# Kernel tuning notes

Hardware: AMD Instinct MI355X
Metric: run time of the kernel (lower is better)

Reference implementation:

```python
import jax, jax.numpy as jnp
import numpy as np


def _conv(x, w, b, pad):
    # x: [N,C,H,W], w: [O,C,kh,kw]
    out = jax.lax.conv_general_dilated(
        x, w, window_strides=(1, 1), padding=[(pad, pad), (pad, pad)],
        dimension_numbers=("NCHW", "OIHW", "NCHW"))
    return out + b[None, :, None, None]


def _deform_conv(x, offset, mask, w, b):
    # Modulated deformable conv (DCNv2), 3x3 kernel, stride 1, pad 1, dilation 1.
    # x: [N,C,H,W], offset: [N,18,H,W] (per-point (dy,dx) pairs), mask: [N,9,H,W]
    N, C, H, W = x.shape
    KK = 9
    off = offset.reshape(N, KK, 2, H, W)
    dy, dx = off[:, :, 0], off[:, :, 1]            # [N,9,H,W]
    k = jnp.arange(3, dtype=x.dtype) - 1.0         # kernel taps -1,0,1
    ky = jnp.repeat(k, 3)                          # row-major 3x3 order
    kx = jnp.tile(k, 3)
    py = dy + ky[None, :, None, None] + jnp.arange(H, dtype=x.dtype)[None, None, :, None]
    px = dx + kx[None, :, None, None] + jnp.arange(W, dtype=x.dtype)[None, None, None, :]
    y0 = jnp.floor(py)
    x0 = jnp.floor(px)
    wy = (py - y0)[..., None]                      # [N,9,H,W,1]
    wx = (px - x0)[..., None]
    x_t = x.transpose(0, 2, 3, 1).reshape(N, H * W, C)  # [N,HW,C]

    def gather(iy, ix):
        valid = ((iy >= 0) & (iy < H) & (ix >= 0) & (ix < W)).astype(x.dtype)
        idx = (jnp.clip(iy, 0, H - 1).astype(jnp.int32) * W
               + jnp.clip(ix, 0, W - 1).astype(jnp.int32)).reshape(N, -1)
        v = jax.vmap(lambda a, i: a[i])(x_t, idx).reshape(N, KK, H, W, C)
        return v * valid[..., None]

    v00 = gather(y0, x0)
    v01 = gather(y0, x0 + 1)
    v10 = gather(y0 + 1, x0)
    v11 = gather(y0 + 1, x0 + 1)
    samp = (v00 * (1 - wy) * (1 - wx) + v01 * (1 - wy) * wx
            + v10 * wy * (1 - wx) + v11 * wy * wx)
    samp = samp * mask[..., None]                  # modulation
    O = w.shape[0]
    out = jnp.einsum("nkhwc,ock->nohw", samp, w.reshape(O, C, KK))
    return out + b[None, :, None, None]


def _res_block(x, w1, b1, w2, b2):
    # ResidualBlock_noBN: x + conv2(relu(conv1(x)))
    return x + _conv(jax.nn.relu(_conv(x, w1, b1, 1)), w2, b2, 1)


def setup_inputs() -> dict:
    key = jax.random.key(0)
    ks = jax.random.split(key, 16)
    f = jnp.float32

    def rn(k, shape, scale):
        return jax.random.normal(k, shape, dtype=f) * scale

    N, C, H, W = 2, 64, 128, 128
    inp = {}
    inp["xd"] = rn(ks[0], (N, 2 * C, H // 2, W // 2), 1.0)
    inp["xl"] = rn(ks[1], (N, C, H, W), 1.0)
    inp["xr"] = rn(ks[2], (N, C, H, W), 1.0)
    inp["up_w"] = rn(ks[3], (C, 2 * C, 2, 2), (2 * C * 4) ** -0.5)
    inp["up_b"] = jnp.zeros((C,), f)
    inp["offl_w"] = rn(ks[4], (27, 3 * C, 3, 3), 0.01 * (3 * C * 9) ** -0.5)
    inp["offl_b"] = jnp.zeros((27,), f)
    inp["dl_w"] = rn(ks[5], (C, C, 3, 3), (C * 9) ** -0.5)
    inp["dl_b"] = jnp.zeros((C,), f)
    inp["offr_w"] = rn(ks[6], (27, 3 * C, 3, 3), 0.01 * (3 * C * 9) ** -0.5)
    inp["offr_b"] = jnp.zeros((27,), f)
    inp["dr_w"] = rn(ks[7], (C, C, 3, 3), (C * 9) ** -0.5)
    inp["dr_b"] = jnp.zeros((C,), f)
    inp["cv_w"] = rn(ks[8], (C, 3 * C, 3, 3), (3 * C * 9) ** -0.5)
    inp["cv_b"] = jnp.zeros((C,), f)
    for i, nm in enumerate(["rb1_w1", "rb1_w2", "rb2_w1", "rb2_w2"]):
        inp[nm] = rn(ks[9 + i], (C, C, 3, 3), (C * 9) ** -0.5)
    for nm in ["rb1_b1", "rb1_b2", "rb2_b1", "rb2_b2"]:
        inp[nm] = jnp.zeros((C,), f)
    return inp


def reference(xd, xl, xr, up_w, up_b, offl_w, offl_b, dl_w, dl_b,
              offr_w, offr_b, dr_w, dr_b, cv_w, cv_b,
              rb1_w1, rb1_b1, rb1_w2, rb1_b2,
              rb2_w1, rb2_b1, rb2_w2, rb2_b2):
    # UP_SAMPLE: nearest x2 upsample, then k=2 conv (pad 0 -> size 2H-1)
    xd = jnp.repeat(jnp.repeat(xd, 2, axis=2), 2, axis=3)
    xd = _conv(xd, up_w, up_b, 0)
    dY = xl.shape[2] - xd.shape[2]
    dX = xl.shape[3] - xd.shape[3]
    xd = jnp.pad(xd, ((0, 0), (0, 0), (dY // 2, dY - dY // 2), (dX // 2, dX - dX // 2)))
    # left deform branch
    ol = _conv(jnp.concatenate([xl, xr, xd], axis=1), offl_w, offl_b, 1)
    off_l = ol[:, :18]                    # cat(o1, o2)
    mask_l = jax.nn.sigmoid(ol[:, 18:])
    xl = _deform_conv(xl, off_l, mask_l, dl_w, dl_b)
    # right deform branch (uses updated xl)
    orr = _conv(jnp.concatenate([xl, xr, xd], axis=1), offr_w, offr_b, 1)
    off_r = orr[:, :18]
    mask_r = jax.nn.sigmoid(orr[:, 18:])
    xr = _deform_conv(xr, off_r, mask_r, dr_w, dr_b)
    # CONV_BLOCK: conv+relu then two residual blocks
    x = jnp.concatenate([xl, xr, xd], axis=1)
    x = jax.nn.relu(_conv(x, cv_w, cv_b, 1))
    x = _res_block(x, rb1_w1, rb1_b1, rb1_w2, rb1_b2)
    x = _res_block(x, rb2_w1, rb2_b1, rb2_w2, rb2_b2)
    return x
```

## Files before the change

### kernel.cpp

```cpp
#include <hip/hip_runtime.h>
#include <math.h>

#define HW 16384

typedef unsigned short u16;
typedef __attribute__((ext_vector_type(8))) short short8;
typedef __attribute__((ext_vector_type(16))) float f32x16;

union U16B {
  uint4 u;
  short8 v;
  u16 s[8];
};

__device__ inline u16 f2b(float f) {
  unsigned u = __float_as_uint(f);
  u += 0x7FFF + ((u >> 16) & 1);
  return (u16)(u >> 16);
}
__device__ inline float b2f(u16 h) {
  return __uint_as_float(((unsigned)h) << 16);
}

__device__ inline u16 pack_frag(const float* __restrict__ w, int Cin, int O,
                                int OT, int d) {
  int j = d & 7;
  int lane = (d >> 3) & 63;
  int rest = d >> 9;
  int ot = rest % OT; rest /= OT;
  int ks = rest & 3; rest >>= 2;
  int kx = rest % 3; rest /= 3;
  int ky = rest % 3; int s = rest / 3;
  int och = ot * 32 + (lane & 31);
  int ch = s * 64 + ks * 16 + ((lane >> 5) << 3) + j;
  if (och >= O) return 0;
  return f2b(w[((size_t)och * Cin + ch) * 9 + ky * 3 + kx]);
}

__device__ inline u16 pack_def(const float* __restrict__ w, int d) {
  int j = d & 7;
  int lane = (d >> 3) & 63;
  int g = d >> 9;
  int ot = g & 1;
  int t = g >> 1;
  int ks = t & 3;
  int k = t >> 2;
  int och = ot * 32 + (lane & 31);
  int c = ks * 16 + ((lane >> 5) << 3) + j;
  return f2b(w[((size_t)och * 64 + c) * 9 + k]);
}

__device__ inline u16 pack_up(const float* __restrict__ w, int d) {
  int j = d & 7;
  int lane = (d >> 3) & 63;
  int g = d >> 9;
  int ot = g & 1;
  int rest = g >> 1;
  int ks = rest & 7;
  int t = rest >> 3;
  int och = ot * 32 + (lane & 31);
  int ci = ks * 16 + ((lane >> 5) << 3) + j;
  return f2b(w[((size_t)och * 128 + ci) * 4 + t]);
}

__global__ __launch_bounds__(256) void setup_kernel(
    const float* __restrict__ dl_w, const float* __restrict__ dr_w,
    const float* __restrict__ up_w, const float* __restrict__ cv_w,
    const float* __restrict__ offl_w, const float* __restrict__ offr_w,
    const float* __restrict__ r1a, const float* __restrict__ r1b,
    const float* __restrict__ r2a, const float* __restrict__ r2b,
    u16* __restrict__ wup, u16* __restrict__ wdl, u16* __restrict__ wdr,
    u16* __restrict__ wcv, u16* __restrict__ wofl, u16* __restrict__ wofr,
    u16* __restrict__ wr1a, u16* __restrict__ wr1b,
    u16* __restrict__ wr2a, u16* __restrict__ wr2b,
    const float* __restrict__ xl, const float* __restrict__ xr,
    u16* __restrict__ xlh, u16* __restrict__ xrh,
    const float* __restrict__ xd, u16* __restrict__ xdh) {
  __shared__ float sT[8448];
  int tid = threadIdx.x;
  int b = blockIdx.x;
  if (b < 1856) {
    int d = b * 256 + tid;
    if (d < 32768) { wup[d] = pack_up(up_w, d); return; }
    d -= 32768;
    if (d < 36864) { wdl[d] = pack_def(dl_w, d); return; }
    d -= 36864;
    if (d < 36864) { wdr[d] = pack_def(dr_w, d); return; }
    d -= 36864;
    if (d < 110592) { wcv[d] = pack_frag(cv_w, 192, 64, 2, d); return; }
    d -= 110592;
    if (d < 55296) { wofl[d] = pack_frag(offl_w, 192, 27, 1, d); return; }
    d -= 55296;
    if (d < 55296) { wofr[d] = pack_frag(offr_w, 192, 27, 1, d); return; }
    d -= 55296;
    if (d < 36864) { wr1a[d] = pack_frag(r1a, 64, 64, 2, d); return; }
    d -= 36864;
    if (d < 36864) { wr1b[d] = pack_frag(r1b, 64, 64, 2, d); return; }
    d -= 36864;
    if (d < 36864) { wr2a[d] = pack_frag(r2a, 64, 64, 2, d); return; }
    d -= 36864;
    if (d < 36864) { wr2b[d] = pack_frag(r2b, 64, 64, 2, d); return; }
    return;
  }
  b -= 1856;
  if (b < 512) {
    int y = b & 127;
    int pid = b >> 7;
    const float* src = (pid >> 1) ? xr : xl;
    u16* dst = (pid >> 1) ? xrh : xlh;
    int n = pid & 1;
#pragma unroll
    for (int i = 0; i < 8; ++i) {
      int q = tid + i * 256;
      int ch = q >> 5, pxq = q & 31;
      float4 v = *(const float4*)(src + ((size_t)(n * 64 + ch)) * HW + y * 128 + pxq * 4);
      *(float4*)&sT[ch * 132 + pxq * 4] = v;
    }
    __syncthreads();
    int px = tid >> 1, half = tid & 1;
    u16* op = dst + (((size_t)(n * 128 + y)) * 128 + px) * 64 + half * 32;
#pragma unroll
    for (int c = 0; c < 4; ++c) {
      uint4 v;
      int ob = (half * 32 + c * 8);
      v.x = (unsigned)f2b(sT[(ob + 0) * 132 + px]) | ((unsigned)f2b(sT[(ob + 1) * 132 + px]) << 16);
      v.y = (unsigned)f2b(sT[(ob + 2) * 132 + px]) | ((unsigned)f2b(sT[(ob + 3) * 132 + px]) << 16);
      v.z = (unsigned)f2b(sT[(ob + 4) * 132 + px]) | ((unsigned)f2b(sT[(ob + 5) * 132 + px]) << 16);
      v.w = (unsigned)f2b(sT[(ob + 6) * 132 + px]) | ((unsigned)f2b(sT[(ob + 7) * 132 + px]) << 16);
      *(uint4*)(op + c * 8) = v;
    }
    return;
  }
  b -= 512;
  {
    int r = b & 63;
    int n = b >> 6;
#pragma unroll
    for (int i = 0; i < 8; ++i) {
      int q = tid + i * 256;
      int ch = q >> 4, col4 = q & 15;
      float4 v = *(const float4*)(xd + ((size_t)(n * 128 + ch) * 64 + r) * 64 + col4 * 4);
      *(float4*)&sT[ch * 66 + col4 * 4] = v;
    }
    __syncthreads();
#pragma unroll
    for (int i = 0; i < 4; ++i) {
      int q = tid + i * 256;
      int col = q >> 4, cho = q & 15;
      uint4 v;
      int cb = cho * 8;
      v.x = (unsigned)f2b(sT[(cb + 0) * 66 + col]) | ((unsigned)f2b(sT[(cb + 1) * 66 + col]) << 16);
      v.y = (unsigned)f2b(sT[(cb + 2) * 66 + col]) | ((unsigned)f2b(sT[(cb + 3) * 66 + col]) << 16);
      v.z = (unsigned)f2b(sT[(cb + 4) * 66 + col]) | ((unsigned)f2b(sT[(cb + 5) * 66 + col]) << 16);
      v.w = (unsigned)f2b(sT[(cb + 6) * 66 + col]) | ((unsigned)f2b(sT[(cb + 7) * 66 + col]) << 16);
      *(uint4*)(xdh + (((size_t)(n * 64 + r)) * 64 + col) * 128 + cb) = v;
    }
  }
}

__global__ __launch_bounds__(1024) void upconv_mf(
    const u16* __restrict__ xdh, const u16* __restrict__ wup,
    const float* __restrict__ bias, u16* __restrict__ outH) {
  __shared__ float s_red[4][3][16][64];
  const int tid = threadIdx.x;
  const int lane = tid & 63;
  const int w = tid >> 6;
  const int p2 = w >> 2;
  const int t = w & 3;
  const int y = blockIdx.x;
  const int n = blockIdx.y;
  const int px = (p2 << 5) + (lane & 31);
  const int h = lane >> 5;

  f32x16 acc0, acc1;
#pragma unroll
  for (int i = 0; i < 16; ++i) { acc0[i] = 0.f; acc1[i] = 0.f; }

  const u16* xb = xdh + ((size_t)n * 64 * 64) * 128;
  const int ty = t >> 1, tx = t & 1;
  const int row = min((y + ty) >> 1, 63);
  const int col = min((px + tx) >> 1, 63);
  const u16* src = xb + ((size_t)(row * 64 + col)) * 128;
#pragma unroll
  for (int ks = 0; ks < 8; ++ks) {
    U16B bf;
    bf.u = *(const uint4*)(src + ks * 16 + h * 8);
    const u16* wp = wup + ((size_t)((t * 8 + ks) * 2)) * 512 + lane * 8;
    U16B a0, a1;
    a0.u = *(const uint4*)wp;
    a1.u = *(const uint4*)(wp + 512);
    acc0 = __builtin_amdgcn_mfma_f32_32x32x16_bf16(a0.v, bf.v, acc0, 0, 0, 0);
    acc1 = __builtin_amdgcn_mfma_f32_32x32x16_bf16(a1.v, bf.v, acc1, 0, 0, 0);
  }

  const bool zero = (y == 127) || (px == 127);
  const size_t pixb = (((size_t)(n * 128 + y)) * 128 + px) * 64;

  if (t != 0) {
#pragma unroll
    for (int i = 0; i < 16; ++i) s_red[p2][t - 1][i][lane] = acc0[i];
  }
  __syncthreads();
  if (t == 0) {
#pragma unroll
    for (int q = 0; q < 4; ++q) {
      int oo = 8 * q + 4 * h;
      float v[4];
#pragma unroll
      for (int r = 0; r < 4; ++r) {
        int i = q * 4 + r;
        float s = acc0[i] + s_red[p2][0][i][lane] + s_red[p2][1][i][lane] +
                  s_red[p2][2][i][lane];
        v[r] = zero ? 0.f : (s + bias[oo + r]);
      }
      ushort4 hh;
      hh.x = f2b(v[0]); hh.y = f2b(v[1]); hh.z = f2b(v[2]); hh.w = f2b(v[3]);
      *(ushort4*)(outH + pixb + oo) = hh;
    }
  }
  __syncthreads();
  if (t != 0) {
#pragma unroll
    for (int i = 0; i < 16; ++i) s_red[p2][t - 1][i][lane] = acc1[i];
  }
  __syncthreads();
  if (t == 0) {
#pragma unroll
    for (int q = 0; q < 4; ++q) {
      int oo = 32 + 8 * q + 4 * h;
      float v[4];
#pragma unroll
      for (int r = 0; r < 4; ++r) {
        int i = q * 4 + r;
        float s = acc1[i] + s_red[p2][0][i][lane] + s_red[p2][1][i][lane] +
                  s_red[p2][2][i][lane];
        v[r] = zero ? 0.f : (s + bias[oo + r]);
      }
      ushort4 hh;
      hh.x = f2b(v[0]); hh.y = f2b(v[1]); hh.z = f2b(v[2]); hh.w = f2b(v[3]);
      *(ushort4*)(outH + pixb + oo) = hh;
    }
  }
}

template <int NSEG>
__global__ __launch_bounds__(1024) void mfconv_s(
    const u16* __restrict__ in0, const u16* __restrict__ in1,
    const u16* __restrict__ in2, const u16* __restrict__ wpk,
    const float* __restrict__ bias, const u16* __restrict__ resh,
    float* __restrict__ outF, u16* __restrict__ outH, int mode) {
  __shared__ __align__(16) unsigned char s_un[49920];
  u16* stg = (u16*)s_un;
  float* s_redf = (float*)s_un;

  const int tid = threadIdx.x;
  const int lane = tid & 63;
  const int w = tid >> 6;
  const int p2 = w >> 2;
  const int kq = w & 3;
  const int y = blockIdx.x;
  const int n = blockIdx.y;
  const int px = (p2 << 5) + (lane & 31);
  const int h = lane >> 5;
  const int gpx = lane >> 3;
  const int gcs = lane & 7;

  auto stg_at = [&](int e, int cg, int p) -> u16* {
    return stg + (((e * 8 + cg) * 130 + p) << 3);
  };

  f32x16 acc0, acc1;
#pragma unroll
  for (int i = 0; i < 16; ++i) { acc0[i] = 0.f; acc1[i] = 0.f; }

  for (int s = 0; s < NSEG; ++s) {
    const u16* sp = (s == 0) ? in0 : ((s == 1) ? in1 : in2);
    const u16* bn = sp + ((size_t)n * 128) * 128 * 64;
    for (int i = w; i < 48; i += 16) {
      int ky = i >> 4, g = i & 15;
      int row = y + ky - 1;
      int ppx = g * 8 + gpx;
      uint4 v = make_uint4(0, 0, 0, 0);
      if ((unsigned)row < 128u)
        v = *(const uint4*)(bn + (size_t)row * (128 * 64) + (size_t)ppx * 64 + gcs * 8);
      *(uint4*)stg_at(ky, gcs, ppx) = v;
    }
    __syncthreads();
#pragma unroll
    for (int ky = 0; ky < 3; ++ky) {
#pragma unroll
      for (int kx = 0; kx < 3; ++kx) {
        int pxc = px + kx - 1;
        bool valid = (unsigned)pxc < 128u;
        int pxcc = min(max(pxc, 0), 127);
        U16B bf;
        bf.u = *(const uint4*)stg_at(ky, kq * 2 + h, pxcc);
        if (!valid) bf.u = make_uint4(0, 0, 0, 0);
        const u16* wp = wpk +
            ((size_t)((((s * 3 + ky) * 3 + kx) * 4 + kq) * 2)) * 512 + lane * 8;
        U16B a0, a1;
        a0.u = *(const uint4*)wp;
        a1.u = *(const uint4*)(wp + 512);
        acc0 = __builtin_amdgcn_mfma_f32_32x32x16_bf16(a0.v, bf.v, acc0, 0, 0, 0);
        acc1 = __builtin_amdgcn_mfma_f32_32x32x16_bf16(a1.v, bf.v, acc1, 0, 0, 0);
      }
    }
    __syncthreads();
  }

  const size_t pixb = ((size_t)(n * 128 + y)) * 128 + px;

  if (kq != 0) {
#pragma unroll
    for (int i = 0; i < 16; ++i)
      s_redf[((p2 * 3 + (kq - 1)) * 16 + i) * 64 + lane] = acc0[i];
  }
  __syncthreads();
  if (kq == 0) {
#pragma unroll
    for (int q = 0; q < 4; ++q) {
      int oo = 8 * q + 4 * h;
      float v[4];
#pragma unroll
      for (int r = 0; r < 4; ++r) {
        int i = q * 4 + r;
        v[r] = acc0[i] + s_redf[((p2 * 3 + 0) * 16 + i) * 64 + lane] +
               s_redf[((p2 * 3 + 1) * 16 + i) * 64 + lane] +
               s_redf[((p2 * 3 + 2) * 16 + i) * 64 + lane] + bias[oo + r];
      }
      if (mode == 1) {
#pragma unroll
        for (int r = 0; r < 4; ++r) v[r] = fmaxf(v[r], 0.f);
      } else if (mode == 3) {
        ushort4 rv = *(const ushort4*)(resh + pixb * 64 + oo);
        v[0] += b2f(rv.x); v[1] += b2f(rv.y); v[2] += b2f(rv.z); v[3] += b2f(rv.w);
      }
      if (outH) {
        ushort4 hh;
        hh.x = f2b(v[0]); hh.y = f2b(v[1]); hh.z = f2b(v[2]); hh.w = f2b(v[3]);
        *(ushort4*)(outH + pixb * 64 + oo) = hh;
      } else {
#pragma unroll
        for (int r = 0; r < 4; ++r)
          outF[((size_t)(n * 64 + oo + r)) * HW + y * 128 + px] = v[r];
      }
    }
  }
  __syncthreads();
  if (kq != 0) {
#pragma unroll
    for (int i = 0; i < 16; ++i)
      s_redf[((p2 * 3 + (kq - 1)) * 16 + i) * 64 + lane] = acc1[i];
  }
  __syncthreads();
  if (kq == 0) {
#pragma unroll
    for (int q = 0; q < 4; ++q) {
      int oo = 32 + 8 * q + 4 * h;
      float v[4];
#pragma unroll
      for (int r = 0; r < 4; ++r) {
        int i = q * 4 + r;
        v[r] = acc1[i] + s_redf[((p2 * 3 + 0) * 16 + i) * 64 + lane] +
               s_redf[((p2 * 3 + 1) * 16 + i) * 64 + lane] +
               s_redf[((p2 * 3 + 2) * 16 + i) * 64 + lane] + bias[oo + r];
      }
      if (mode == 1) {
#pragma unroll
        for (int r = 0; r < 4; ++r) v[r] = fmaxf(v[r], 0.f);
      } else if (mode == 3) {
        ushort4 rv = *(const ushort4*)(resh + pixb * 64 + oo);
        v[0] += b2f(rv.x); v[1] += b2f(rv.y); v[2] += b2f(rv.z); v[3] += b2f(rv.w);
      }
      if (outH) {
        ushort4 hh;
        hh.x = f2b(v[0]); hh.y = f2b(v[1]); hh.z = f2b(v[2]); hh.w = f2b(v[3]);
        *(ushort4*)(outH + pixb * 64 + oo) = hh;
      } else {
#pragma unroll
        for (int r = 0; r < 4; ++r)
          outF[((size_t)(n * 64 + oo + r)) * HW + y * 128 + px] = v[r];
      }
    }
  }
}

__global__ __launch_bounds__(512) void rbfuse(
    const u16* __restrict__ in, const u16* __restrict__ w1,
    const float* __restrict__ b1, const u16* __restrict__ w2,
    const float* __restrict__ b2, float* __restrict__ outF,
    u16* __restrict__ outH) {
  __shared__ __align__(16) u16 ring[3][8][128][8];
  __shared__ __align__(16) u16 mid[3][8][128][8];
  const int tid = threadIdx.x;
  const int lane = tid & 63;
  const int w = tid >> 6;
  const int p2 = w >> 1;
  const int ot = w & 1;
  const int y = blockIdx.x;
  const int n = blockIdx.y;
  const int px = (p2 << 5) + (lane & 31);
  const int h = lane >> 5;
  const int gpx = lane >> 3;
  const int gcs = lane & 7;
  const u16* bn = in + ((size_t)n * 128) * 128 * 64;

  auto stage_row = [&](int r) {
    int sl = ((r % 3) + 3) % 3;
    for (int i = w; i < 16; i += 8) {
      int ppx = i * 8 + gpx;
      uint4 v = make_uint4(0, 0, 0, 0);
      if ((unsigned)r < 128u)
        v = *(const uint4*)(bn + (size_t)r * (128 * 64) + (size_t)ppx * 64 + gcs * 8);
      *(uint4*)&ring[sl][gcs][ppx][0] = v;
    }
  };

  auto conv1_row = [&](int rr, int r) {
    if ((unsigned)r >= 128u) {
      ushort4 z = make_ushort4(0, 0, 0, 0);
#pragma unroll
      for (int q = 0; q < 4; ++q)
        *(ushort4*)&mid[rr][ot * 4 + q][px][4 * h] = z;
      return;
    }
    f32x16 acc;
#pragma unroll
    for (int i = 0; i < 16; ++i) acc[i] = 0.f;
#pragma unroll
    for (int ky = 0; ky < 3; ++ky) {
      int sr = r - 1 + ky;
      int sl = ((sr % 3) + 3) % 3;
#pragma unroll
      for (int kx = 0; kx < 3; ++kx) {
        int pxc = px + kx - 1;
        bool valid = (unsigned)pxc < 128u;
        int pxcc = min(max(pxc, 0), 127);
#pragma unroll
        for (int kq = 0; kq < 4; ++kq) {
          U16B bf;
          bf.u = *(const uint4*)&ring[sl][kq * 2 + h][pxcc][0];
          if (!valid) bf.u = make_uint4(0, 0, 0, 0);
          U16B a;
          a.u = *(const uint4*)(w1 +
                ((size_t)(((ky * 3 + kx) * 4 + kq) * 2 + ot)) * 512 + lane * 8);
          acc = __builtin_amdgcn_mfma_f32_32x32x16_bf16(a.v, bf.v, acc, 0, 0, 0);
        }
      }
    }
#pragma unroll
    for (int q = 0; q < 4; ++q) {
      int oo = ot * 32 + 8 * q + 4 * h;
      ushort4 hh;
      hh.x = f2b(fmaxf(acc[q * 4 + 0] + b1[oo + 0], 0.f));
      hh.y = f2b(fmaxf(acc[q * 4 + 1] + b1[oo + 1], 0.f));
      hh.z = f2b(fmaxf(acc[q * 4 + 2] + b1[oo + 2], 0.f));
      hh.w = f2b(fmaxf(acc[q * 4 + 3] + b1[oo + 3], 0.f));
      *(ushort4*)&mid[rr][ot * 4 + q][px][4 * h] = hh;
    }
  };

  stage_row(y - 2);
  stage_row(y - 1);
  stage_row(y);
  __syncthreads();
  conv1_row(0, y - 1);
  __syncthreads();
  stage_row(y + 1);
  __syncthreads();
  conv1_row(1, y);
  __syncthreads();
  stage_row(y + 2);
  __syncthreads();
  conv1_row(2, y + 1);
  __syncthreads();

  f32x16 acc;
#pragma unroll
  for (int i = 0; i < 16; ++i) acc[i] = 0.f;
#pragma unroll
  for (int ky = 0; ky < 3; ++ky) {
#pragma unroll
    for (int kx = 0; kx < 3; ++kx) {
      int pxc = px + kx - 1;
      bool valid = (unsigned)pxc < 128u;
      int pxcc = min(max(pxc, 0), 127);
#pragma unroll
      for (int kq = 0; kq < 4; ++kq) {
        U16B bf;
        bf.u = *(const uint4*)&mid[ky][kq * 2 + h][pxcc][0];
        if (!valid) bf.u = make_uint4(0, 0, 0, 0);
        U16B a;
        a.u = *(const uint4*)(w2 +
              ((size_t)(((ky * 3 + kx) * 4 + kq) * 2 + ot)) * 512 + lane * 8);
        acc = __builtin_amdgcn_mfma_f32_32x32x16_bf16(a.v, bf.v, acc, 0, 0, 0);
      }
    }
  }

  const int ysl = y % 3;
  const size_t pixb = ((size_t)(n * 128 + y)) * 128 + px;
#pragma unroll
  for (int q = 0; q < 4; ++q) {
    int oo = ot * 32 + 8 * q + 4 * h;
    ushort4 rv = *(const ushort4*)&ring[ysl][ot * 4 + q][px][4 * h];
    float v[4];
    v[0] = acc[q * 4 + 0] + b2[oo + 0] + b2f(rv.x);
    v[1] = acc[q * 4 + 1] + b2[oo + 1] + b2f(rv.y);
    v[2] = acc[q * 4 + 2] + b2[oo + 2] + b2f(rv.z);
    v[3] = acc[q * 4 + 3] + b2[oo + 3] + b2f(rv.w);
    if (outH) {
      ushort4 hh;
      hh.x = f2b(v[0]); hh.y = f2b(v[1]); hh.z = f2b(v[2]); hh.w = f2b(v[3]);
      *(ushort4*)(outH + pixb * 64 + oo) = hh;
    } else {
#pragma unroll
      for (int r = 0; r < 4; ++r)
        outF[((size_t)(n * 64 + oo + r)) * HW + y * 128 + px] = v[r];
    }
  }
}

__global__ __launch_bounds__(512) void deform_fused(
    const u16* __restrict__ in0, const u16* __restrict__ in1,
    const u16* __restrict__ in2, const u16* __restrict__ woff,
    const float* __restrict__ boff, const u16* __restrict__ xh,
    const u16* __restrict__ wdef, const float* __restrict__ bdef,
    u16* __restrict__ outH) {
  __shared__ float s_off[27][64];
  __shared__ __align__(16) unsigned char s_un[30720];
  u16* stg = (u16*)s_un;
  float* s_redf = (float*)s_un;

  const int tid = threadIdx.x;
  const int lane = tid & 63;
  const int w = tid >> 6;
  const int p2 = w >> 2;
  const int kq = w & 3;
  const int y = blockIdx.x >> 1;
  const int hx0 = (blockIdx.x & 1) << 6;
  const int n = blockIdx.y;
  const int lp = (p2 << 5) + (lane & 31);
  const int h = lane >> 5;
  const int gpx = lane >> 3;
  const int gcs = lane & 7;

  auto stg_at = [&](int e, int cg, int p) -> u16* {
    return stg + (((e * 8 + cg) * 80 + p) << 3);
  };

  f32x16 acc;
#pragma unroll
  for (int i = 0; i < 16; ++i) acc[i] = 0.f;

  for (int s = 0; s < 3; ++s) {
    const u16* sp = (s == 0) ? in0 : ((s == 1) ? in1 : in2);
    const u16* bn = sp + ((size_t)n * 128) * 128 * 64;
    for (int i = w; i < 30; i += 8) {
      int ky = i / 10, g = i % 10;
      int row = y + ky - 1;
      int ppx = hx0 - 8 + g * 8 + gpx;
      uint4 v = make_uint4(0, 0, 0, 0);
      if ((unsigned)row < 128u && (unsigned)ppx < 128u)
        v = *(const uint4*)(bn + (size_t)row * (128 * 64) + (size_t)ppx * 64 + gcs * 8);
      *(uint4*)stg_at(ky, gcs, g * 8 + gpx) = v;
    }
    __syncthreads();
#pragma unroll
    for (int ky = 0; ky < 3; ++ky) {
#pragma unroll
      for (int kx = 0; kx < 3; ++kx) {
        U16B bf;
        bf.u = *(const uint4*)stg_at(ky, kq * 2 + h, lp + 7 + kx);
        U16B a;
        a.u = *(const uint4*)(woff +
              ((size_t)(((s * 3 + ky) * 3 + kx) * 4 + kq)) * 512 + lane * 8);
        acc = __builtin_amdgcn_mfma_f32_32x32x16_bf16(a.v, bf.v, acc, 0, 0, 0);
      }
    }
    __syncthreads();
  }

  if (kq != 0) {
#pragma unroll
    for (int i = 0; i < 16; ++i)
      s_redf[((p2 * 3 + (kq - 1)) * 16 + i) * 64 + lane] = acc[i];
  }
  __syncthreads();
  if (kq == 0) {
#pragma unroll
    for (int q = 0; q < 4; ++q) {
#pragma unroll
      for (int r = 0; r < 4; ++r) {
        int och = 8 * q + 4 * h + r;
        if (och < 27) {
          int i = q * 4 + r;
          float v = acc[i] + s_redf[((p2 * 3 + 0) * 16 + i) * 64 + lane] +
                    s_redf[((p2 * 3 + 1) * 16 + i) * 64 + lane] +
                    s_redf[((p2 * 3 + 2) * 16 + i) * 64 + lane] + boff[och];
          if (och >= 18) v = 1.f / (1.f + expf(-v));
          s_off[och][lp] = v;
        }
      }
    }
  }
  __syncthreads();

  f32x16 acc0, acc1;
#pragma unroll
  for (int i = 0; i < 16; ++i) { acc0[i] = 0.f; acc1[i] = 0.f; }

  const u16* xb = xh + ((size_t)n * HW) * 64;

  for (int tc = 0; tc < 3; ++tc) {
    for (int i = w; i < 24; i += 8) {
      int tt = i >> 3, g = i & 7;
      int t = tc * 3 + tt;
      int ppx = g * 8 + gpx;
      int gx = hx0 + ppx;
      int ky = t / 3 - 1, kx = t % 3 - 1;
      float dy = s_off[2 * t][ppx];
      float dx = s_off[2 * t + 1][ppx];
      float m = s_off[18 + t][ppx];
      float py = dy + (float)(y + ky);
      float pxf = dx + (float)(gx + kx);
      float fy = floorf(py), fxx = floorf(pxf);
      float wy = py - fy, wx = pxf - fxx;
      int iy0 = (int)fy, ix0 = (int)fxx;
      bool vy0 = (unsigned)iy0 < 128u, vy1 = (unsigned)(iy0 + 1) < 128u;
      bool vx0 = (unsigned)ix0 < 128u, vx1 = (unsigned)(ix0 + 1) < 128u;
      float omwy = 1.f - wy, omwx = 1.f - wx;
      float f00 = (vy0 && vx0) ? omwy * omwx * m : 0.f;
      float f01 = (vy0 && vx1) ? omwy * wx * m : 0.f;
      float f10 = (vy1 && vx0) ? wy * omwx * m : 0.f;
      float f11 = (vy1 && vx1) ? wy * wx * m : 0.f;
      int y0c = min(max(iy0, 0), 127), y1c = min(max(iy0 + 1, 0), 127);
      int x0c = min(max(ix0, 0), 127), x1c = min(max(ix0 + 1, 0), 127);
      U16B v00, v01, v10, v11;
      v00.u = *(const uint4*)(xb + ((size_t)(y0c * 128 + x0c)) * 64 + gcs * 8);
      v01.u = *(const uint4*)(xb + ((size_t)(y0c * 128 + x1c)) * 64 + gcs * 8);
      v10.u = *(const uint4*)(xb + ((size_t)(y1c * 128 + x0c)) * 64 + gcs * 8);
      v11.u = *(const uint4*)(xb + ((size_t)(y1c * 128 + x1c)) * 64 + gcs * 8);
      unsigned dw[4];
#pragma unroll
      for (int jj = 0; jj < 4; ++jj) {
        float s0 = f00 * b2f(v00.s[2 * jj]) + f01 * b2f(v01.s[2 * jj]) +
                   f10 * b2f(v10.s[2 * jj]) + f11 * b2f(v11.s[2 * jj]);
        float s1 = f00 * b2f(v00.s[2 * jj + 1]) + f01 * b2f(v01.s[2 * jj + 1]) +
                   f10 * b2f(v10.s[2 * jj + 1]) + f11 * b2f(v11.s[2 * jj + 1]);
        dw[jj] = (unsigned)f2b(s0) | ((unsigned)f2b(s1) << 16);
      }
      *(uint4*)stg_at(tt, gcs, ppx) = make_uint4(dw[0], dw[1], dw[2], dw[3]);
    }
    __syncthreads();
#pragma unroll
    for (int tt = 0; tt < 3; ++tt) {
      int t = tc * 3 + tt;
      U16B bf;
      bf.u = *(const uint4*)stg_at(tt, kq * 2 + h, lp);
      const u16* wp = wdef + ((size_t)((t * 4 + kq) * 2)) * 512 + lane * 8;
      U16B a0, a1;
      a0.u = *(const uint4*)wp;
      a1.u = *(const uint4*)(wp + 512);
      acc0 = __builtin_amdgcn_mfma_f32_32x32x16_bf16(a0.v, bf.v, acc0, 0, 0, 0);
      acc1 = __builtin_amdgcn_mfma_f32_32x32x16_bf16(a1.v, bf.v, acc1, 0, 0, 0);
    }
    __syncthreads();
  }

  const size_t pixb = (((size_t)(n * 128 + y)) * 128 + hx0 + lp) * 64;
  if (kq != 0) {
#pragma unroll
    for (int i = 0; i < 16; ++i)
      s_redf[((p2 * 3 + (kq - 1)) * 16 + i) * 64 + lane] = acc0[i];
  }
  __syncthreads();
  if (kq == 0) {
#pragma unroll
    for (int q = 0; q < 4; ++q) {
      int oo = 8 * q + 4 * h;
      float v[4];
#pragma unroll
      for (int r = 0; r < 4; ++r) {
        int i = q * 4 + r;
        v[r] = acc0[i] + s_redf[((p2 * 3 + 0) * 16 + i) * 64 + lane] +
               s_redf[((p2 * 3 + 1) * 16 + i) * 64 + lane] +
               s_redf[((p2 * 3 + 2) * 16 + i) * 64 + lane] + bdef[oo + r];
      }
      ushort4 hh;
      hh.x = f2b(v[0]); hh.y = f2b(v[1]); hh.z = f2b(v[2]); hh.w = f2b(v[3]);
      *(ushort4*)(outH + pixb + oo) = hh;
    }
  }
  __syncthreads();
  if (kq != 0) {
#pragma unroll
    for (int i = 0; i < 16; ++i)
      s_redf[((p2 * 3 + (kq - 1)) * 16 + i) * 64 + lane] = acc1[i];
  }
  __syncthreads();
  if (kq == 0) {
#pragma unroll
    for (int q = 0; q < 4; ++q) {
      int oo = 32 + 8 * q + 4 * h;
      float v[4];
#pragma unroll
      for (int r = 0; r < 4; ++r) {
        int i = q * 4 + r;
        v[r] = acc1[i] + s_redf[((p2 * 3 + 0) * 16 + i) * 64 + lane] +
               s_redf[((p2 * 3 + 1) * 16 + i) * 64 + lane] +
               s_redf[((p2 * 3 + 2) * 16 + i) * 64 + lane] + bdef[oo + r];
      }
      ushort4 hh;
      hh.x = f2b(v[0]); hh.y = f2b(v[1]); hh.z = f2b(v[2]); hh.w = f2b(v[3]);
      *(ushort4*)(outH + pixb + oo) = hh;
    }
  }
}

extern "C" void kernel_launch(void* const* d_in, const int* in_sizes, int n_in,
                              void* d_out, int out_size, void* d_ws, size_t ws_size,
                              hipStream_t stream) {
  const float* xd = (const float*)d_in[0];
  const float* xl = (const float*)d_in[1];
  const float* xr = (const float*)d_in[2];
  const float* up_w = (const float*)d_in[3];
  const float* up_b = (const float*)d_in[4];
  const float* offl_w = (const float*)d_in[5];
  const float* offl_b = (const float*)d_in[6];
  const float* dl_w = (const float*)d_in[7];
  const float* dl_b = (const float*)d_in[8];
  const float* offr_w = (const float*)d_in[9];
  const float* offr_b = (const float*)d_in[10];
  const float* dr_w = (const float*)d_in[11];
  const float* dr_b = (const float*)d_in[12];
  const float* cv_w = (const float*)d_in[13];
  const float* cv_b = (const float*)d_in[14];
  const float* rb1_w1 = (const float*)d_in[15];
  const float* rb1_w2 = (const float*)d_in[16];
  const float* rb2_w1 = (const float*)d_in[17];
  const float* rb2_w2 = (const float*)d_in[18];
  const float* rb1_b1 = (const float*)d_in[19];
  const float* rb1_b2 = (const float*)d_in[20];
  const float* rb2_b1 = (const float*)d_in[21];
  const float* rb2_b2 = (const float*)d_in[22];

  float* ws = (float*)d_ws;
  u16* hb = (u16*)(ws + 1769472);
  u16* xlh = hb;
  u16* xrh = hb + 2097152;
  u16* xdph = hb + 4194304;
  u16* xl2h = hb + 6291456;
  u16* xr2h = hb + 8388608;
  u16* t0h = hb + 10485760;
  u16* t1h = hb + 12582912;
  u16* t2h = hb + 14680064;
  u16* t3h = hb + 16777216;
  u16* xdh = hb + 18874368;
  u16* wcv = hb + 19922944;
  u16* wofl = hb + 20033536;
  u16* wofr = hb + 20088832;
  u16* wr1a = hb + 20144128;
  u16* wr1b = hb + 20180992;
  u16* wr2a = hb + 20217856;
  u16* wr2b = hb + 20254720;
  u16* wdl = hb + 20291584;
  u16* wdr = hb + 20328448;
  u16* wup = hb + 20365312;
  float* outp = (float*)d_out;

  hipLaunchKernelGGL(setup_kernel, dim3(2496), dim3(256), 0, stream,
                     dl_w, dr_w, up_w, cv_w, offl_w, offr_w, rb1_w1, rb1_w2,
                     rb2_w1, rb2_w2, wup, wdl, wdr, wcv, wofl, wofr, wr1a,
                     wr1b, wr2a, wr2b, xl, xr, xlh, xrh, xd, xdh);
  hipLaunchKernelGGL(upconv_mf, dim3(128, 2), dim3(1024), 0, stream,
                     xdh, wup, up_b, xdph);
  hipLaunchKernelGGL(deform_fused, dim3(256, 2), dim3(512), 0, stream,
                     xlh, xrh, xdph, wofl, offl_b, xlh, wdl, dl_b, xl2h);
  hipLaunchKernelGGL(deform_fused, dim3(256, 2), dim3(512), 0, stream,
                     xl2h, xrh, xdph, wofr, offr_b, xrh, wdr, dr_b, xr2h);
  hipLaunchKernelGGL(mfconv_s<3>, dim3(128, 2), dim3(1024), 0, stream,
                     xl2h, xr2h, xdph, wcv, cv_b, (const u16*)nullptr,
                     (float*)nullptr, t0h, 1);
  hipLaunchKernelGGL(rbfuse, dim3(128, 2), dim3(512), 0, stream,
                     t0h, wr1a, rb1_b1, wr1b, rb1_b2, (float*)nullptr, t2h);
  hipLaunchKernelGGL(rbfuse, dim3(128, 2), dim3(512), 0, stream,
                     t2h, wr2a, rb2_b1, wr2b, rb2_b2, outp, (u16*)nullptr);
}
```

Before: 131.6 us.

## Software-pipeline global loads in deform_fused offset conv and bilinear gather

Register-prefetches the next input segment for the offset convolution while MFMAs run on the current staged segment. In the deformable sampling phase, the bilinear gather loads for the next tap chunk are issued before the current chunk is blended and multiplied, using double-buffered register arrays. Launch bounds are set to one block per SM so the compiler can spend the extra registers. The aim is to hide global-memory latency behind compute, at the cost of higher register pressure and possibly lower occupancy.

```diff
diff --git a/kernel.cpp b/kernel.cpp
--- a/kernel.cpp
+++ b/kernel.cpp
@@ -521,7 +521,7 @@
   }
 }
 
-__global__ __launch_bounds__(512) void deform_fused(
+__global__ __launch_bounds__(512, 1) void deform_fused(
     const u16* __restrict__ in0, const u16* __restrict__ in1,
     const u16* __restrict__ in2, const u16* __restrict__ woff,
     const float* __restrict__ boff, const u16* __restrict__ xh,
@@ -553,19 +553,41 @@
 #pragma unroll
   for (int i = 0; i < 16; ++i) acc[i] = 0.f;
 
-  for (int s = 0; s < 3; ++s) {
+  uint4 pre[4];
+  auto ld_seg = [&](int s) {
     const u16* sp = (s == 0) ? in0 : ((s == 1) ? in1 : in2);
     const u16* bn = sp + ((size_t)n * 128) * 128 * 64;
-    for (int i = w; i < 30; i += 8) {
-      int ky = i / 10, g = i % 10;
-      int row = y + ky - 1;
-      int ppx = hx0 - 8 + g * 8 + gpx;
+#pragma unroll
+    for (int u = 0; u < 4; ++u) {
+      int i = w + u * 8;
       uint4 v = make_uint4(0, 0, 0, 0);
-      if ((unsigned)row < 128u && (unsigned)ppx < 128u)
-        v = *(const uint4*)(bn + (size_t)row * (128 * 64) + (size_t)ppx * 64 + gcs * 8);
-      *(uint4*)stg_at(ky, gcs, g * 8 + gpx) = v;
-    }
+      if (i < 30) {
+        int ky = i / 10, g = i % 10;
+        int row = y + ky - 1;
+        int ppx = hx0 - 8 + g * 8 + gpx;
+        if ((unsigned)row < 128u && (unsigned)ppx < 128u)
+          v = *(const uint4*)(bn + (size_t)row * (128 * 64) + (size_t)ppx * 64 + gcs * 8);
+      }
+      pre[u] = v;
+    }
+  };
+  auto wr_seg = [&]() {
+#pragma unroll
+    for (int u = 0; u < 4; ++u) {
+      int i = w + u * 8;
+      if (i < 30) {
+        int ky = i / 10, g = i % 10;
+        *(uint4*)stg_at(ky, gcs, g * 8 + gpx) = pre[u];
+      }
+    }
+  };
+
+  ld_seg(0);
+#pragma unroll
+  for (int s = 0; s < 3; ++s) {
+    wr_seg();
     __syncthreads();
+    if (s < 2) ld_seg(s + 1);
 #pragma unroll
     for (int ky = 0; ky < 3; ++ky) {
 #pragma unroll
@@ -611,48 +633,61 @@
   for (int i = 0; i < 16; ++i) { acc0[i] = 0.f; acc1[i] = 0.f; }
 
   const u16* xb = xh + ((size_t)n * HW) * 64;
-
-  for (int tc = 0; tc < 3; ++tc) {
-    for (int i = w; i < 24; i += 8) {
-      int tt = i >> 3, g = i & 7;
-      int t = tc * 3 + tt;
-      int ppx = g * 8 + gpx;
-      int gx = hx0 + ppx;
+  const int ppx2 = w * 8 + gpx;
+  const int gx2 = hx0 + ppx2;
+
+  float cfA[3][4], cfB[3][4];
+  uint4 glA[3][4], glB[3][4];
+
+  auto prep = [&](int tc, float (&cf)[3][4], uint4 (&gl)[3][4]) {
+#pragma unroll
+    for (int u = 0; u < 3; ++u) {
+      int t = tc * 3 + u;
       int ky = t / 3 - 1, kx = t % 3 - 1;
-      float dy = s_off[2 * t][ppx];
-      float dx = s_off[2 * t + 1][ppx];
-      float m = s_off[18 + t][ppx];
+      float dy = s_off[2 * t][ppx2];
+      float dx = s_off[2 * t + 1][ppx2];
+      float m = s_off[18 + t][ppx2];
       float py = dy + (float)(y + ky);
-      float pxf = dx + (float)(gx + kx);
+      float pxf = dx + (float)(gx2 + kx);
       float fy = floorf(py), fxx = floorf(pxf);
       float wy = py - fy, wx = pxf - fxx;
       int iy0 = (int)fy, ix0 = (int)fxx;
       bool vy0 = (unsigned)iy0 < 128u, vy1 = (unsigned)(iy0 + 1) < 128u;
       bool vx0 = (unsigned)ix0 < 128u, vx1 = (unsigned)(ix0 + 1) < 128u;
       float omwy = 1.f - wy, omwx = 1.f - wx;
-      float f00 = (vy0 && vx0) ? omwy * omwx * m : 0.f;
-      float f01 = (vy0 && vx1) ? omwy * wx * m : 0.f;
-      float f10 = (vy1 && vx0) ? wy * omwx * m : 0.f;
-      float f11 = (vy1 && vx1) ? wy * wx * m : 0.f;
+      cf[u][0] = (vy0 && vx0) ? omwy * omwx * m : 0.f;
+      cf[u][1] = (vy0 && vx1) ? omwy * wx * m : 0.f;
+      cf[u][2] = (vy1 && vx0) ? wy * omwx * m : 0.f;
+      cf[u][3] = (vy1 && vx1) ? wy * wx * m : 0.f;
       int y0c = min(max(iy0, 0), 127), y1c = min(max(iy0 + 1, 0), 127);
       int x0c = min(max(ix0, 0), 127), x1c = min(max(ix0 + 1, 0), 127);
-      U16B v00, v01, v10, v11;
-      v00.u = *(const uint4*)(xb + ((size_t)(y0c * 128 + x0c)) * 64 + gcs * 8);
-      v01.u = *(const uint4*)(xb + ((size_t)(y0c * 128 + x1c)) * 64 + gcs * 8);
-      v10.u = *(const uint4*)(xb + ((size_t)(y1c * 128 + x0c)) * 64 + gcs * 8);
-      v11.u = *(const uint4*)(xb + ((size_t)(y1c * 128 + x1c)) * 64 + gcs * 8);
+      gl[u][0] = *(const uint4*)(xb + ((size_t)(y0c * 128 + x0c)) * 64 + gcs * 8);
+      gl[u][1] = *(const uint4*)(xb + ((size_t)(y0c * 128 + x1c)) * 64 + gcs * 8);
+      gl[u][2] = *(const uint4*)(xb + ((size_t)(y1c * 128 + x0c)) * 64 + gcs * 8);
+      gl[u][3] = *(const uint4*)(xb + ((size_t)(y1c * 128 + x1c)) * 64 + gcs * 8);
+    }
+  };
+
+  auto blendw = [&](float (&cf)[3][4], uint4 (&gl)[3][4]) {
+#pragma unroll
+    for (int u = 0; u < 3; ++u) {
+      U16B q0, q1, q2, q3;
+      q0.u = gl[u][0]; q1.u = gl[u][1]; q2.u = gl[u][2]; q3.u = gl[u][3];
+      float f00 = cf[u][0], f01 = cf[u][1], f10 = cf[u][2], f11 = cf[u][3];
       unsigned dw[4];
 #pragma unroll
       for (int jj = 0; jj < 4; ++jj) {
-        float s0 = f00 * b2f(v00.s[2 * jj]) + f01 * b2f(v01.s[2 * jj]) +
-                   f10 * b2f(v10.s[2 * jj]) + f11 * b2f(v11.s[2 * jj]);
-        float s1 = f00 * b2f(v00.s[2 * jj + 1]) + f01 * b2f(v01.s[2 * jj + 1]) +
-                   f10 * b2f(v10.s[2 * jj + 1]) + f11 * b2f(v11.s[2 * jj + 1]);
+        float s0 = f00 * b2f(q0.s[2 * jj]) + f01 * b2f(q1.s[2 * jj]) +
+                   f10 * b2f(q2.s[2 * jj]) + f11 * b2f(q3.s[2 * jj]);
+        float s1 = f00 * b2f(q0.s[2 * jj + 1]) + f01 * b2f(q1.s[2 * jj + 1]) +
+                   f10 * b2f(q2.s[2 * jj + 1]) + f11 * b2f(q3.s[2 * jj + 1]);
         dw[jj] = (unsigned)f2b(s0) | ((unsigned)f2b(s1) << 16);
       }
-      *(uint4*)stg_at(tt, gcs, ppx) = make_uint4(dw[0], dw[1], dw[2], dw[3]);
-    }
-    __syncthreads();
+      *(uint4*)stg_at(u, gcs, ppx2) = make_uint4(dw[0], dw[1], dw[2], dw[3]);
+    }
+  };
+
+  auto mfma_chunk = [&](int tc) {
 #pragma unroll
     for (int tt = 0; tt < 3; ++tt) {
       int t = tc * 3 + tt;
@@ -665,8 +700,23 @@
       acc0 = __builtin_amdgcn_mfma_f32_32x32x16_bf16(a0.v, bf.v, acc0, 0, 0, 0);
       acc1 = __builtin_amdgcn_mfma_f32_32x32x16_bf16(a1.v, bf.v, acc1, 0, 0, 0);
     }
-    __syncthreads();
-  }
+  };
+
+  prep(0, cfA, glA);
+  prep(1, cfB, glB);
+  blendw(cfA, glA);
+  __syncthreads();
+  mfma_chunk(0);
+  __syncthreads();
+  prep(2, cfA, glA);
+  blendw(cfB, glB);
+  __syncthreads();
+  mfma_chunk(1);
+  __syncthreads();
+  blendw(cfA, glA);
+  __syncthreads();
+  mfma_chunk(2);
+  __syncthreads();
 
   const size_t pixb = (((size_t)(n * 128 + y)) * 128 + hx0 + lp) * 64;
   if (kq != 0) {
```

Result: slower. 154.0 us (+17.0%).
